# Kernel optimization log

Hardware: AMD Instinct MI355X
Metric: run time of the kernel (lower is better)

## Reference

```python
import jax, jax.numpy as jnp
import numpy as np

B, N, E, H, NE = 8, 512, 512, 8, 16384
DH = E // H
SCALE = DH ** -0.5
EPS = 1e-5


def _layernorm(x, g, b):
    mu = jnp.mean(x, axis=-1, keepdims=True)
    var = jnp.var(x, axis=-1, keepdims=True)
    return (x - mu) / jnp.sqrt(var + EPS) * g + b


def setup_inputs() -> dict:
    key = jax.random.key(0)
    ks = jax.random.split(key, 24)
    s = 0.02
    return {
        "x": jax.random.normal(ks[0], (B, N, E), jnp.float32),
        "edge_attr": jax.random.normal(ks[1], (NE, E), jnp.float32),
        "Wq": jax.random.normal(ks[2], (E, E), jnp.float32) * s,
        "bq": jnp.zeros((E,), jnp.float32),
        "Wk": jax.random.normal(ks[3], (E, E), jnp.float32) * s,
        "bk": jnp.zeros((E,), jnp.float32),
        "Wv": jax.random.normal(ks[4], (E, E), jnp.float32) * s,
        "bv": jnp.zeros((E,), jnp.float32),
        "Wo": jax.random.normal(ks[5], (E, E), jnp.float32) * s,
        "bo": jnp.zeros((E,), jnp.float32),
        "dist_table": jax.random.normal(ks[6], (100, H), jnp.float32),
        "We": jax.random.normal(ks[7], (H, E), jnp.float32) * s,
        "be": jnp.zeros((H,), jnp.float32),
        "W1": jax.random.normal(ks[8], (4 * E, E), jnp.float32) * s,
        "b1": jnp.zeros((4 * E,), jnp.float32),
        "W2": jax.random.normal(ks[9], (E, 4 * E), jnp.float32) * s,
        "b2": jnp.zeros((E,), jnp.float32),
        "g1": jnp.ones((E,), jnp.float32),
        "beta1": jnp.zeros((E,), jnp.float32),
        "g2": jnp.ones((E,), jnp.float32),
        "beta2": jnp.zeros((E,), jnp.float32),
        "edge_index": jax.random.randint(ks[10], (2, NE), 0, N, jnp.int64),
        "distance_matrix": jax.random.randint(ks[11], (B, N, N), 0, 100, jnp.int32),
    }


def reference(x, edge_attr, Wq, bq, Wk, bk, Wv, bv, Wo, bo, dist_table, We, be,
              W1, b1, W2, b2, g1, beta1, g2, beta2, edge_index, distance_matrix):
    residual = x
    h = _layernorm(x, g1, beta1)
    # projections -> [B, H, N, DH]
    def proj(W, b):
        return (h @ W.T + b).reshape(B, N, H, DH).transpose(0, 2, 1, 3)
    q, k, v = proj(Wq, bq), proj(Wk, bk), proj(Wv, bv)
    attn = jnp.einsum('bhnd,bhmd->bhnm', q, k) * SCALE
    # distance-encoding gather: [B,N,N] -> [B,N,N,H] -> [B,H,N,N]
    d_idx = jnp.clip(distance_matrix, 0, 99)
    attn = attn + dist_table[d_idx].transpose(0, 3, 1, 2)
    # per-edge scatter-add bias (duplicates accumulate, matching sequential loop)
    edge_enc = (edge_attr @ We.T + be).T  # [H, NE]
    src, tgt = edge_index[0], edge_index[1]
    edge_bias = jnp.zeros((H, N, N), attn.dtype).at[:, src, tgt].add(edge_enc)
    attn = attn + edge_bias[None]
    attn = jax.nn.softmax(attn, axis=-1)
    out = jnp.einsum('bhnm,bhmd->bhnd', attn, v)
    out = out.transpose(0, 2, 1, 3).reshape(B, N, E)
    out = out @ Wo.T + bo
    x1 = residual + out
    h2 = _layernorm(x1, g2, beta2)
    ffn = jax.nn.gelu(h2 @ W1.T + b1, approximate=False) @ W2.T + b2
    return x1 + ffn
```

## Files before the change

kernel.cpp:

```cpp
#include <hip/hip_runtime.h>
#include <cstdint>
#include <cstddef>

#define B_  8
#define N_  512
#define E_  512
#define H_  8
#define DH_ 64
#define NE_ 16384
#define QT  64

using u16   = unsigned short;
using bf16x8 = __attribute__((ext_vector_type(8))) __bf16;
using u16x8  = __attribute__((ext_vector_type(8))) unsigned short;
using f32x4  = __attribute__((ext_vector_type(4))) float;

__device__ __forceinline__ u16 f2b(float f) {
  unsigned u = __builtin_bit_cast(unsigned, f);
  u += 0x7fffu + ((u >> 16) & 1u);
  return (u16)(u >> 16);
}

__device__ __forceinline__ bf16x8 ld_frag(const u16* p) {
  return __builtin_bit_cast(bf16x8, *(const u16x8*)p);
}

__device__ __forceinline__ void gld_lds16(const u16* g, u16* l) {
  __builtin_amdgcn_global_load_lds(
      (const __attribute__((address_space(1))) unsigned*)(g),
      (__attribute__((address_space(3))) unsigned*)(l), 16, 0, 0);
}

__device__ __forceinline__ void gemm_core_128x128(
    const u16* __restrict__ At, int lda,
    const u16* __restrict__ Bt, int ldb, int K,
    u16* ldsA, u16* ldsB, f32x4 (&acc)[4][4]) {
  const int tid  = threadIdx.x;
  const int wid  = tid >> 6, lane = tid & 63;
  const int wr   = wid >> 1, wc = wid & 1;
  const int qd   = lane >> 4, r = lane & 15;
  const int mrow = tid >> 2, k0 = (tid & 3) * 8;
  const int wbase = wid << 9;
  for (int kt = 0; kt < K; kt += 32) {
    __syncthreads();
    gld_lds16(&At[(size_t)mrow*lda + kt + k0],        ldsA + wbase);
    gld_lds16(&At[(size_t)(mrow+64)*lda + kt + k0],   ldsA + 64*32 + wbase);
    gld_lds16(&Bt[(size_t)mrow*ldb + kt + k0],        ldsB + wbase);
    gld_lds16(&Bt[(size_t)(mrow+64)*ldb + kt + k0],   ldsB + 64*32 + wbase);
    __syncthreads();
    bf16x8 af[4], bfv[4];
#pragma unroll
    for (int i = 0; i < 4; ++i) af[i] = ld_frag(&ldsA[(wr*64 + i*16 + r)*32 + qd*8]);
#pragma unroll
    for (int j = 0; j < 4; ++j) bfv[j] = ld_frag(&ldsB[(wc*64 + j*16 + r)*32 + qd*8]);
#pragma unroll
    for (int i = 0; i < 4; ++i)
#pragma unroll
      for (int j = 0; j < 4; ++j)
        acc[i][j] = __builtin_amdgcn_mfma_f32_16x16x32_bf16(af[i], bfv[j], acc[i][j], 0, 0, 0);
  }
}

template <int EPI>
__global__ __launch_bounds__(256) void gemm_epi(
    const u16* __restrict__ A, const u16* __restrict__ W,
    const float* __restrict__ bias, const float* __restrict__ res,
    float* __restrict__ outf, u16* __restrict__ outb, int Kd, int Nd) {
  __shared__ u16 ldsA[128*32];
  __shared__ u16 ldsB[128*32];
  const int bx = blockIdx.x, by = blockIdx.y;
  f32x4 acc[4][4] = {};
  gemm_core_128x128(A + (size_t)bx*128*Kd, Kd, W + (size_t)by*128*Kd, Kd, Kd,
                    ldsA, ldsB, acc);
  const int tid = threadIdx.x, wid = tid>>6, lane = tid&63;
  const int wr = wid>>1, wc = wid&1, qd = lane>>4, r = lane&15;
#pragma unroll
  for (int i = 0; i < 4; ++i) {
#pragma unroll
    for (int j = 0; j < 4; ++j) {
      const int grow = bx*128 + wr*64 + i*16 + qd*4;
      const int gcol = by*128 + wc*64 + j*16 + r;
      const float bb = bias[gcol];
#pragma unroll
      for (int rg = 0; rg < 4; ++rg) {
        float v = acc[i][j][rg] + bb;
        const size_t idx = (size_t)(grow + rg)*Nd + gcol;
        if constexpr (EPI == 0) {
          outb[idx] = f2b(v);
        } else if constexpr (EPI == 1) {
          outf[idx] = v + res[idx];
        } else {
          v = 0.5f * v * (1.0f + erff(v * 0.70710678118f));
          outb[idx] = f2b(v);
        }
      }
    }
  }
}

__global__ __launch_bounds__(256) void gemm_splitk_k(
    const u16* __restrict__ A, const u16* __restrict__ W,
    float* __restrict__ part, int Kd, int Nd, int Ks) {
  __shared__ u16 ldsA[128*32];
  __shared__ u16 ldsB[128*32];
  const int bx = blockIdx.x, by = blockIdx.y, s = blockIdx.z;
  f32x4 acc[4][4] = {};
  gemm_core_128x128(A + (size_t)bx*128*Kd + (size_t)s*Ks, Kd,
                    W + (size_t)by*128*Kd + (size_t)s*Ks, Kd, Ks,
                    ldsA, ldsB, acc);
  const int tid = threadIdx.x, wid = tid>>6, lane = tid&63;
  const int wr = wid>>1, wc = wid&1, qd = lane>>4, r = lane&15;
  float* po = part + (size_t)s*(B_*N_)*Nd;
#pragma unroll
  for (int i = 0; i < 4; ++i) {
#pragma unroll
    for (int j = 0; j < 4; ++j) {
      const int grow = bx*128 + wr*64 + i*16 + qd*4;
      const int gcol = by*128 + wc*64 + j*16 + r;
#pragma unroll
      for (int rg = 0; rg < 4; ++rg)
        po[(size_t)(grow + rg)*Nd + gcol] = acc[i][j][rg];
    }
  }
}

template <int S>
__global__ __launch_bounds__(256) void splitk_reduce_k(
    const float* __restrict__ part, const float* __restrict__ bias,
    const float* __restrict__ res, float* __restrict__ out) {
  const size_t base = ((size_t)blockIdx.x*256 + threadIdx.x) * 4;
  float4 v = *(const float4*)&res[base];
  const int col = (int)(base & (E_-1));
  const float4 bb = *(const float4*)&bias[col];
  v.x += bb.x; v.y += bb.y; v.z += bb.z; v.w += bb.w;
#pragma unroll
  for (int s = 0; s < S; ++s) {
    const float4 p = *(const float4*)&part[(size_t)s*(B_*N_*E_) + base];
    v.x += p.x; v.y += p.y; v.z += p.z; v.w += p.w;
  }
  *(float4*)&out[base] = v;
}

__global__ __launch_bounds__(256) void qkv_gemm_k(
    const u16* __restrict__ A,
    const u16* __restrict__ Wqb, const u16* __restrict__ Wkb, const u16* __restrict__ Wvb,
    const float* __restrict__ bq, const float* __restrict__ bk, const float* __restrict__ bv,
    u16* __restrict__ qo, u16* __restrict__ ko, u16* __restrict__ vo) {
  __shared__ u16 ldsA[128*32];
  __shared__ u16 ldsB[128*32];
  const int bx = blockIdx.x, by = blockIdx.y, z = blockIdx.z;
  const u16*   W    = z == 0 ? Wqb : (z == 1 ? Wkb : Wvb);
  const float* bias = z == 0 ? bq  : (z == 1 ? bk  : bv);
  u16*         outb = z == 0 ? qo  : (z == 1 ? ko  : vo);
  f32x4 acc[4][4] = {};
  gemm_core_128x128(A + (size_t)bx*128*E_, E_, W + (size_t)by*128*E_, E_, E_,
                    ldsA, ldsB, acc);
  const int tid = threadIdx.x, wid = tid>>6, lane = tid&63;
  const int wr = wid>>1, wc = wid&1, qd = lane>>4, r = lane&15;
#pragma unroll
  for (int i = 0; i < 4; ++i) {
#pragma unroll
    for (int j = 0; j < 4; ++j) {
      const int grow = bx*128 + wr*64 + i*16 + qd*4;
      const int gcol = by*128 + wc*64 + j*16 + r;
      const float bb = bias[gcol];
#pragma unroll
      for (int rg = 0; rg < 4; ++rg)
        outb[(size_t)(grow + rg)*E_ + gcol] = f2b(acc[i][j][rg] + bb);
    }
  }
}

__global__ __launch_bounds__(256) void flash_attn_k(
    const u16* __restrict__ qm, const u16* __restrict__ km, const u16* __restrict__ vm,
    const float* __restrict__ dtab, const int* __restrict__ Dm,
    const float* __restrict__ ebias, u16* __restrict__ outb) {
  __shared__ u16 sQ[QT*72];
  __shared__ u16 sK[128*72];
  __shared__ u16 sP[QT*136];
  __shared__ u16 sVt[64*136];
  __shared__ float sDtab[100*H_];
  __shared__ float sMax[2][QT], sSum[2][QT], sM[QT], sL[QT], sAlpha[QT];

  const int bx = blockIdx.x;
  const int bz = blockIdx.y; const int b = bz>>3, h = bz&7;
  const int n0 = bx*QT;
  const int tid = threadIdx.x, wid = tid>>6, lane = tid&63;
  const int wr = wid>>1, wc = wid&1, qd = lane>>4, r = lane&15;

  {
    const u16* Qg = qm + ((size_t)(b*N_ + n0))*E_ + h*DH_;
#pragma unroll
    for (int it = 0; it < 2; ++it) {
      int idx = it*256 + tid;
      int row = idx>>3, d0 = (idx&7)*8;
      *(u16x8*)&sQ[row*72 + d0] = *(const u16x8*)&Qg[(size_t)row*E_ + d0];
    }
    for (int idx = tid; idx < 100*H_; idx += 256) sDtab[idx] = dtab[idx];
    if (tid < QT) { sM[tid] = -3.0e38f; sL[tid] = 0.f; }
  }

  f32x4 accO[2][2] = {};
  const int*   Db = Dm + (size_t)b*N_*N_;
  const float* Eb = ebias + (size_t)h*N_*N_;

  for (int mc = 0; mc < N_; mc += 128) {
    __syncthreads();
    {
      const u16* Kg = km + ((size_t)(b*N_ + mc))*E_ + h*DH_;
#pragma unroll
      for (int it = 0; it < 4; ++it) {
        int idx = it*256 + tid;
        int row = idx>>3, d0 = (idx&7)*8;
        *(u16x8*)&sK[row*72 + d0] = *(const u16x8*)&Kg[(size_t)row*E_ + d0];
      }
      const u16* Vg = vm + ((size_t)(b*N_ + mc))*E_ + h*DH_;
#pragma unroll
      for (int it = 0; it < 4; ++it) {
        int idx = it*256 + tid;
        int m = idx>>3, d0 = (idx&7)*8;
        u16x8 u = *(const u16x8*)&Vg[(size_t)m*E_ + d0];
#pragma unroll
        for (int e = 0; e < 8; ++e) sVt[(d0+e)*136 + m] = u[e];
      }
    }
    __syncthreads();
    f32x4 accS[2][4] = {};
#pragma unroll
    for (int ks = 0; ks < 2; ++ks) {
      bf16x8 af[2], bfv[4];
#pragma unroll
      for (int i = 0; i < 2; ++i) af[i] = ld_frag(&sQ[(wr*32 + i*16 + r)*72 + ks*32 + qd*8]);
#pragma unroll
      for (int j = 0; j < 4; ++j) bfv[j] = ld_frag(&sK[(wc*64 + j*16 + r)*72 + ks*32 + qd*8]);
#pragma unroll
      for (int i = 0; i < 2; ++i)
#pragma unroll
        for (int j = 0; j < 4; ++j)
          accS[i][j] = __builtin_amdgcn_mfma_f32_16x16x32_bf16(af[i], bfv[j], accS[i][j], 0, 0, 0);
    }
    float rmax[2][4];
#pragma unroll
    for (int i = 0; i < 2; ++i)
#pragma unroll
      for (int rg = 0; rg < 4; ++rg) rmax[i][rg] = -3.0e38f;
#pragma unroll
    for (int i = 0; i < 2; ++i) {
      const int n = n0 + wr*32 + i*16 + qd*4;
#pragma unroll
      for (int j = 0; j < 4; ++j) {
        const int m = mc + wc*64 + j*16 + r;
#pragma unroll
        for (int rg = 0; rg < 4; ++rg) {
          int di = Db[(size_t)(n+rg)*N_ + m];
          di = di < 0 ? 0 : (di > 99 ? 99 : di);
          float v = accS[i][j][rg]*0.125f + sDtab[di*H_ + h] + Eb[(size_t)(n+rg)*N_ + m];
          accS[i][j][rg] = v;
          rmax[i][rg] = fmaxf(rmax[i][rg], v);
        }
      }
    }
#pragma unroll
    for (int i = 0; i < 2; ++i)
#pragma unroll
      for (int rg = 0; rg < 4; ++rg) {
        float v = rmax[i][rg];
        v = fmaxf(v, __shfl_xor(v, 1)); v = fmaxf(v, __shfl_xor(v, 2));
        v = fmaxf(v, __shfl_xor(v, 4)); v = fmaxf(v, __shfl_xor(v, 8));
        if (r == 0) sMax[wc][wr*32 + i*16 + qd*4 + rg] = v;
      }
    __syncthreads();
    if (tid < QT) {
      float mcx  = fmaxf(sMax[0][tid], sMax[1][tid]);
      float mnew = fmaxf(sM[tid], mcx);
      sAlpha[tid] = __expf(sM[tid] - mnew);
      sM[tid] = mnew;
    }
    __syncthreads();
    float rsum[2][4];
#pragma unroll
    for (int i = 0; i < 2; ++i) {
      const int lr0 = wr*32 + i*16 + qd*4;
#pragma unroll
      for (int rg = 0; rg < 4; ++rg) {
        const float mrow = sM[lr0 + rg];
        float partial = 0.f;
#pragma unroll
        for (int j = 0; j < 4; ++j) {
          float p = __expf(accS[i][j][rg] - mrow);
          partial += p;
          sP[(lr0+rg)*136 + wc*64 + j*16 + r] = f2b(p);
        }
        rsum[i][rg] = partial;
        const float a = sAlpha[lr0 + rg];
#pragma unroll
        for (int jj = 0; jj < 2; ++jj) accO[i][jj][rg] *= a;
      }
    }
#pragma unroll
    for (int i = 0; i < 2; ++i)
#pragma unroll
      for (int rg = 0; rg < 4; ++rg) {
        float v = rsum[i][rg];
        v += __shfl_xor(v, 1); v += __shfl_xor(v, 2);
        v += __shfl_xor(v, 4); v += __shfl_xor(v, 8);
        if (r == 0) sSum[wc][wr*32 + i*16 + qd*4 + rg] = v;
      }
    __syncthreads();
    if (tid < QT) sL[tid] = sL[tid]*sAlpha[tid] + sSum[0][tid] + sSum[1][tid];
    __syncthreads();
#pragma unroll
    for (int ks = 0; ks < 4; ++ks) {
      bf16x8 af[2], bfv[2];
#pragma unroll
      for (int i = 0; i < 2; ++i) af[i] = ld_frag(&sP[(wr*32 + i*16 + r)*136 + ks*32 + qd*8]);
#pragma unroll
      for (int jj = 0; jj < 2; ++jj) bfv[jj] = ld_frag(&sVt[(wc*32 + jj*16 + r)*136 + ks*32 + qd*8]);
#pragma unroll
      for (int i = 0; i < 2; ++i)
#pragma unroll
        for (int jj = 0; jj < 2; ++jj)
          accO[i][jj] = __builtin_amdgcn_mfma_f32_16x16x32_bf16(af[i], bfv[jj], accO[i][jj], 0, 0, 0);
    }
  }
#pragma unroll
  for (int i = 0; i < 2; ++i) {
    const int lr0 = wr*32 + i*16 + qd*4;
#pragma unroll
    for (int jj = 0; jj < 2; ++jj) {
      const int d = wc*32 + jj*16 + r;
#pragma unroll
      for (int rg = 0; rg < 4; ++rg) {
        const float inv = 1.0f / sL[lr0 + rg];
        outb[((size_t)(b*N_ + n0 + lr0 + rg))*E_ + h*DH_ + d] = f2b(accO[i][jj][rg] * inv);
      }
    }
  }
}

__global__ __launch_bounds__(256) void layernorm_k(
    const float* __restrict__ x, const float* __restrict__ g,
    const float* __restrict__ be, u16* __restrict__ outb) {
  const int row = blockIdx.x, t = threadIdx.x;
  const float* xr = x + (size_t)row*E_;
  const float v0 = xr[t], v1 = xr[t+256];
  float s = v0 + v1, ss = v0*v0 + v1*v1;
  for (int o = 32; o; o >>= 1) { s += __shfl_down(s, o); ss += __shfl_down(ss, o); }
  __shared__ float rs[4], rss[4];
  const int wid = t>>6, lane = t&63;
  if (!lane) { rs[wid] = s; rss[wid] = ss; }
  __syncthreads();
  s  = rs[0]+rs[1]+rs[2]+rs[3];
  ss = rss[0]+rss[1]+rss[2]+rss[3];
  const float mu   = s * (1.0f/E_);
  const float var  = ss * (1.0f/E_) - mu*mu;
  const float rstd = rsqrtf(var + 1e-5f);
  outb[(size_t)row*E_ + t]       = f2b((v0-mu)*rstd*g[t] + be[t]);
  outb[(size_t)row*E_ + t + 256] = f2b((v1-mu)*rstd*g[t+256] + be[t+256]);
}

#define SEG0 32768
#define SEG1 65536
#define SEG2 98304
#define SEG3 131072
#define SEG4 262144
#define SEG5 393216
__global__ __launch_bounds__(256) void cvt_all_k(
    const float* __restrict__ Wq, const float* __restrict__ Wk,
    const float* __restrict__ Wv, const float* __restrict__ Wo,
    const float* __restrict__ W1, const float* __restrict__ W2,
    u16* __restrict__ wq_b, u16* __restrict__ wk_b, u16* __restrict__ wv_b,
    u16* __restrict__ wo_b, u16* __restrict__ w1_b, u16* __restrict__ w2_b) {
  const int i = blockIdx.x*256 + threadIdx.x;
  const float* src; u16* dst; int base;
  if      (i < SEG0) { src = Wq; dst = wq_b; base = 0; }
  else if (i < SEG1) { src = Wk; dst = wk_b; base = SEG0; }
  else if (i < SEG2) { src = Wv; dst = wv_b; base = SEG1; }
  else if (i < SEG3) { src = Wo; dst = wo_b; base = SEG2; }
  else if (i < SEG4) { src = W1; dst = w1_b; base = SEG3; }
  else               { src = W2; dst = w2_b; base = SEG4; }
  const int li = i - base;
  const float4 f0 = *(const float4*)&src[(size_t)li*8];
  const float4 f1 = *(const float4*)&src[(size_t)li*8 + 4];
  u16x8 u;
  u[0]=f2b(f0.x); u[1]=f2b(f0.y); u[2]=f2b(f0.z); u[3]=f2b(f0.w);
  u[4]=f2b(f1.x); u[5]=f2b(f1.y); u[6]=f2b(f1.z); u[7]=f2b(f1.w);
  *(u16x8*)&dst[(size_t)li*8] = u;
}

__global__ __launch_bounds__(256) void edge_enc_scatter_k(
    const float* __restrict__ ea, const float* __restrict__ We,
    const float* __restrict__ be, const int* __restrict__ ei,
    float* __restrict__ eb) {
  const int wglob = (blockIdx.x*256 + threadIdx.x) >> 6;
  const int lane  = threadIdx.x & 63;
  float w[8][8];
#pragma unroll
  for (int h = 0; h < 8; ++h) {
    const float4 f0 = *(const float4*)&We[h*E_ + lane*8];
    const float4 f1 = *(const float4*)&We[h*E_ + lane*8 + 4];
    w[h][0]=f0.x; w[h][1]=f0.y; w[h][2]=f0.z; w[h][3]=f0.w;
    w[h][4]=f1.x; w[h][5]=f1.y; w[h][6]=f1.z; w[h][7]=f1.w;
  }
  const float beh = (lane < 8) ? be[lane] : 0.f;
#pragma unroll 1
  for (int t = 0; t < NE_/2048; ++t) {
    const int e = wglob*(NE_/2048) + t;
    const float* ar = ea + (size_t)e*E_;
    const float4 a0 = *(const float4*)&ar[lane*8];
    const float4 a1 = *(const float4*)&ar[lane*8 + 4];
    const float a[8] = {a0.x,a0.y,a0.z,a0.w,a1.x,a1.y,a1.z,a1.w};
    float acc[8];
#pragma unroll
    for (int h = 0; h < 8; ++h) {
      float s = 0.f;
#pragma unroll
      for (int j = 0; j < 8; ++j) s += a[j]*w[h][j];
      acc[h] = s;
    }
#pragma unroll
    for (int h = 0; h < 8; ++h) {
      float v = acc[h];
      v += __shfl_xor(v, 1);  v += __shfl_xor(v, 2);  v += __shfl_xor(v, 4);
      v += __shfl_xor(v, 8);  v += __shfl_xor(v, 16); v += __shfl_xor(v, 32);
      acc[h] = v;
    }
    float myv = acc[0];
#pragma unroll
    for (int h = 1; h < 8; ++h) myv = (lane == h) ? acc[h] : myv;
    if (lane < 8) {
      const int s2 = ei[e], t2 = ei[NE_ + e];
      atomicAdd(&eb[((size_t)lane*N_ + s2)*N_ + t2], myv + beh);
    }
  }
}

extern "C" void kernel_launch(void* const* d_in, const int* in_sizes, int n_in,
                              void* d_out, int out_size, void* d_ws, size_t ws_size,
                              hipStream_t stream) {
  const float* x     = (const float*)d_in[0];
  const float* ea    = (const float*)d_in[1];
  const float* Wq    = (const float*)d_in[2];
  const float* bq    = (const float*)d_in[3];
  const float* Wk    = (const float*)d_in[4];
  const float* bk    = (const float*)d_in[5];
  const float* Wv    = (const float*)d_in[6];
  const float* bv    = (const float*)d_in[7];
  const float* Wo    = (const float*)d_in[8];
  const float* bo    = (const float*)d_in[9];
  const float* dtab  = (const float*)d_in[10];
  const float* We    = (const float*)d_in[11];
  const float* be    = (const float*)d_in[12];
  const float* W1    = (const float*)d_in[13];
  const float* b1    = (const float*)d_in[14];
  const float* W2    = (const float*)d_in[15];
  const float* b2    = (const float*)d_in[16];
  const float* g1    = (const float*)d_in[17];
  const float* bet1  = (const float*)d_in[18];
  const float* g2    = (const float*)d_in[19];
  const float* bet2  = (const float*)d_in[20];
  const int*   eidx  = (const int*)d_in[21];
  const int*   Dmat  = (const int*)d_in[22];
  float* out = (float*)d_out;

  char* ws = (char*)d_ws;
  size_t off = 0;
  auto alloc = [&](size_t bytes) -> void* {
    void* p = ws + off;
    off += (bytes + 255) & ~(size_t)255;
    return p;
  };
  u16* wq_b = (u16*)alloc((size_t)E_*E_*2);
  u16* wk_b = (u16*)alloc((size_t)E_*E_*2);
  u16* wv_b = (u16*)alloc((size_t)E_*E_*2);
  u16* wo_b = (u16*)alloc((size_t)E_*E_*2);
  u16* w1_b = (u16*)alloc((size_t)4*E_*E_*2);
  u16* w2_b = (u16*)alloc((size_t)4*E_*E_*2);
  u16* h_b  = (u16*)alloc((size_t)B_*N_*E_*2);
  u16* q_b  = (u16*)alloc((size_t)B_*N_*E_*2);
  u16* k_b  = (u16*)alloc((size_t)B_*N_*E_*2);
  u16* v_b  = (u16*)alloc((size_t)B_*N_*E_*2);
  float* ebias = (float*)alloc((size_t)H_*N_*N_*4);
  float* x1    = (float*)alloc((size_t)B_*N_*E_*4);
  u16*   h2_b  = (u16*)alloc((size_t)B_*N_*E_*2);
  u16*   mid_b = (u16*)alloc((size_t)B_*N_*4*E_*2);
  float* part  = (float*)alloc((size_t)4*B_*N_*E_*4);
  u16*   ao_b  = h_b;

  const int M = B_*N_;

  cvt_all_k<<<dim3(SEG5/256), 256, 0, stream>>>(
      Wq, Wk, Wv, Wo, W1, W2, wq_b, wk_b, wv_b, wo_b, w1_b, w2_b);

  layernorm_k<<<dim3(M), 256, 0, stream>>>(x, g1, bet1, h_b);

  qkv_gemm_k<<<dim3(M/128, E_/128, 3), 256, 0, stream>>>(
      h_b, wq_b, wk_b, wv_b, bq, bk, bv, q_b, k_b, v_b);

  hipMemsetAsync(ebias, 0, (size_t)H_*N_*N_*4, stream);
  edge_enc_scatter_k<<<dim3(512), 256, 0, stream>>>(ea, We, be, eidx, ebias);

  flash_attn_k<<<dim3(N_/QT, B_*H_), 256, 0, stream>>>(
      q_b, k_b, v_b, dtab, Dmat, ebias, ao_b);

  gemm_splitk_k<<<dim3(M/128, E_/128, 2), 256, 0, stream>>>(
      ao_b, wo_b, part, E_, E_, E_/2);
  splitk_reduce_k<2><<<dim3(M*E_/1024), 256, 0, stream>>>(part, bo, x, x1);

  layernorm_k<<<dim3(M), 256, 0, stream>>>(x1, g2, bet2, h2_b);

  gemm_epi<2><<<dim3(M/128, 4*E_/128), 256, 0, stream>>>(h2_b, w1_b, b1, nullptr, nullptr, mid_b, E_, 4*E_);

  gemm_splitk_k<<<dim3(M/128, E_/128, 4), 256, 0, stream>>>(
      mid_b, w2_b, part, 4*E_, E_, E_);
  splitk_reduce_k<4><<<dim3(M*E_/1024), 256, 0, stream>>>(part, b2, x1, out);
}
```

Measured before the change: 280.1 us.

## Fuse layernorms into neighbours and restructure flash attention loads and softmax state

Merges the weight conversion and first layernorm into one launch, and fuses the Wo split-K reduction with the second layernorm. Flash attention now loads Q/K through direct global-to-LDS copies in a k-split layout and prefetches distance and edge-bias values into registers before the barrier. It keeps the running max and sum per thread in registers, removing two block barriers per tile, and staggers the V-transpose and P stores to reduce LDS bank conflicts. This adds register pressure (32 prefetched values per thread), which may lower occupancy.

```diff
diff --git a/kernel.cpp b/kernel.cpp
--- a/kernel.cpp
+++ b/kernel.cpp
@@ -141,6 +141,42 @@
   *(float4*)&out[base] = v;
 }
 
+__device__ __forceinline__ void ln_store(
+    float v0, float v1, const float* __restrict__ g,
+    const float* __restrict__ be, u16* __restrict__ outb, int row, int t) {
+  float s = v0 + v1, ss = v0*v0 + v1*v1;
+  for (int o = 32; o; o >>= 1) { s += __shfl_down(s, o); ss += __shfl_down(ss, o); }
+  __shared__ float rs[4], rss[4];
+  const int wid = t>>6, lane = t&63;
+  if (!lane) { rs[wid] = s; rss[wid] = ss; }
+  __syncthreads();
+  s  = rs[0]+rs[1]+rs[2]+rs[3];
+  ss = rss[0]+rss[1]+rss[2]+rss[3];
+  const float mu   = s * (1.0f/E_);
+  const float var  = ss * (1.0f/E_) - mu*mu;
+  const float rstd = rsqrtf(var + 1e-5f);
+  outb[(size_t)row*E_ + t]       = f2b((v0-mu)*rstd*g[t] + be[t]);
+  outb[(size_t)row*E_ + t + 256] = f2b((v1-mu)*rstd*g[t+256] + be[t+256]);
+}
+
+__global__ __launch_bounds__(256) void splitk_reduce_ln_k(
+    const float* __restrict__ part, const float* __restrict__ bias,
+    const float* __restrict__ res, float* __restrict__ x1,
+    const float* __restrict__ g, const float* __restrict__ be,
+    u16* __restrict__ h2b) {
+  const int row = blockIdx.x, t = threadIdx.x;
+  const size_t base = (size_t)row*E_;
+  float v0 = res[base + t]       + bias[t];
+  float v1 = res[base + t + 256] + bias[t + 256];
+#pragma unroll
+  for (int s = 0; s < 2; ++s) {
+    v0 += part[(size_t)s*(B_*N_*E_) + base + t];
+    v1 += part[(size_t)s*(B_*N_*E_) + base + t + 256];
+  }
+  x1[base + t] = v0; x1[base + t + 256] = v1;
+  ln_store(v0, v1, g, be, h2b, row, t);
+}
+
 __global__ __launch_bounds__(256) void qkv_gemm_k(
     const u16* __restrict__ A,
     const u16* __restrict__ Wqb, const u16* __restrict__ Wkb, const u16* __restrict__ Wvb,
@@ -175,53 +211,75 @@
     const u16* __restrict__ qm, const u16* __restrict__ km, const u16* __restrict__ vm,
     const float* __restrict__ dtab, const int* __restrict__ Dm,
     const float* __restrict__ ebias, u16* __restrict__ outb) {
-  __shared__ u16 sQ[QT*72];
-  __shared__ u16 sK[128*72];
-  __shared__ u16 sP[QT*136];
+  __shared__ u16 sQ[2*64*32];
+  __shared__ u16 sK[2*128*32];
+  __shared__ u16 sP[64*136];
   __shared__ u16 sVt[64*136];
-  __shared__ float sDtab[100*H_];
-  __shared__ float sMax[2][QT], sSum[2][QT], sM[QT], sL[QT], sAlpha[QT];
+  __shared__ float sDt[104];
+  __shared__ float sMax[2][64], sSum[2][64];
 
   const int bx = blockIdx.x;
   const int bz = blockIdx.y; const int b = bz>>3, h = bz&7;
   const int n0 = bx*QT;
   const int tid = threadIdx.x, wid = tid>>6, lane = tid&63;
   const int wr = wid>>1, wc = wid&1, qd = lane>>4, r = lane&15;
-
-  {
-    const u16* Qg = qm + ((size_t)(b*N_ + n0))*E_ + h*DH_;
-#pragma unroll
-    for (int it = 0; it < 2; ++it) {
-      int idx = it*256 + tid;
-      int row = idx>>3, d0 = (idx&7)*8;
-      *(u16x8*)&sQ[row*72 + d0] = *(const u16x8*)&Qg[(size_t)row*E_ + d0];
-    }
-    for (int idx = tid; idx < 100*H_; idx += 256) sDtab[idx] = dtab[idx];
-    if (tid < QT) { sM[tid] = -3.0e38f; sL[tid] = 0.f; }
-  }
-
-  f32x4 accO[2][2] = {};
+  const int lrow = lane>>2, lk = (lane&3)*8;
+
+  const u16* Qg = qm + ((size_t)(b*N_ + n0))*E_ + h*DH_;
+  const u16* Kg = km + (size_t)b*N_*E_ + h*DH_;
+  const u16* Vg = vm + (size_t)b*N_*E_ + h*DH_;
   const int*   Db = Dm + (size_t)b*N_*N_;
   const float* Eb = ebias + (size_t)h*N_*N_;
 
+  {
+#pragma unroll
+    for (int ks = 0; ks < 2; ++ks)
+      gld_lds16(&Qg[(size_t)(wid*16 + lrow)*E_ + ks*32 + lk],
+                sQ + ks*2048 + wid*16*32);
+    for (int idx = tid; idx < 100; idx += 256) sDt[idx] = dtab[idx*H_ + h];
+  }
+
+  float mI[2][4], lI[2][4], alph[2][4];
+#pragma unroll
+  for (int i = 0; i < 2; ++i)
+#pragma unroll
+    for (int rg = 0; rg < 4; ++rg) { mI[i][rg] = -3.0e38f; lI[i][rg] = 0.f; }
+  f32x4 accO[2][2] = {};
+
   for (int mc = 0; mc < N_; mc += 128) {
+    int   dpre[2][4][4];
+    float epre[2][4][4];
+#pragma unroll
+    for (int i = 0; i < 2; ++i) {
+      const int nb = n0 + wr*32 + i*16 + qd*4;
+#pragma unroll
+      for (int j = 0; j < 4; ++j) {
+        const int m = mc + wc*64 + j*16 + r;
+#pragma unroll
+        for (int rg = 0; rg < 4; ++rg) {
+          dpre[i][j][rg] = Db[(size_t)(nb+rg)*N_ + m];
+          epre[i][j][rg] = Eb[(size_t)(nb+rg)*N_ + m];
+        }
+      }
+    }
     __syncthreads();
-    {
-      const u16* Kg = km + ((size_t)(b*N_ + mc))*E_ + h*DH_;
-#pragma unroll
-      for (int it = 0; it < 4; ++it) {
-        int idx = it*256 + tid;
-        int row = idx>>3, d0 = (idx&7)*8;
-        *(u16x8*)&sK[row*72 + d0] = *(const u16x8*)&Kg[(size_t)row*E_ + d0];
-      }
-      const u16* Vg = vm + ((size_t)(b*N_ + mc))*E_ + h*DH_;
-#pragma unroll
-      for (int it = 0; it < 4; ++it) {
-        int idx = it*256 + tid;
-        int m = idx>>3, d0 = (idx&7)*8;
-        u16x8 u = *(const u16x8*)&Vg[(size_t)m*E_ + d0];
-#pragma unroll
-        for (int e = 0; e < 8; ++e) sVt[(d0+e)*136 + m] = u[e];
+#pragma unroll
+    for (int t = 0; t < 2; ++t) {
+      const int row0 = wid*32 + t*16;
+#pragma unroll
+      for (int ks = 0; ks < 2; ++ks)
+        gld_lds16(&Kg[(size_t)(mc + row0 + lrow)*E_ + ks*32 + lk],
+                  sK + ks*4096 + row0*32);
+    }
+#pragma unroll
+    for (int it = 0; it < 4; ++it) {
+      const int idx = it*256 + tid;
+      const int m = idx>>3, d0 = (idx&7)*8;
+      const u16x8 u = *(const u16x8*)&Vg[(size_t)(mc+m)*E_ + d0];
+#pragma unroll
+      for (int e = 0; e < 8; ++e) {
+        const int pe = (e + (d0>>3)) & 7;
+        sVt[(d0+pe)*136 + m] = u[pe];
       }
     }
     __syncthreads();
@@ -230,9 +288,11 @@
     for (int ks = 0; ks < 2; ++ks) {
       bf16x8 af[2], bfv[4];
 #pragma unroll
-      for (int i = 0; i < 2; ++i) af[i] = ld_frag(&sQ[(wr*32 + i*16 + r)*72 + ks*32 + qd*8]);
-#pragma unroll
-      for (int j = 0; j < 4; ++j) bfv[j] = ld_frag(&sK[(wc*64 + j*16 + r)*72 + ks*32 + qd*8]);
+      for (int i = 0; i < 2; ++i)
+        af[i] = ld_frag(&sQ[ks*2048 + (wr*32 + i*16 + r)*32 + qd*8]);
+#pragma unroll
+      for (int j = 0; j < 4; ++j)
+        bfv[j] = ld_frag(&sK[ks*4096 + (wc*64 + j*16 + r)*32 + qd*8]);
 #pragma unroll
       for (int i = 0; i < 2; ++i)
 #pragma unroll
@@ -245,21 +305,17 @@
 #pragma unroll
       for (int rg = 0; rg < 4; ++rg) rmax[i][rg] = -3.0e38f;
 #pragma unroll
-    for (int i = 0; i < 2; ++i) {
-      const int n = n0 + wr*32 + i*16 + qd*4;
-#pragma unroll
-      for (int j = 0; j < 4; ++j) {
-        const int m = mc + wc*64 + j*16 + r;
+    for (int i = 0; i < 2; ++i)
+#pragma unroll
+      for (int j = 0; j < 4; ++j)
 #pragma unroll
         for (int rg = 0; rg < 4; ++rg) {
-          int di = Db[(size_t)(n+rg)*N_ + m];
+          int di = dpre[i][j][rg];
           di = di < 0 ? 0 : (di > 99 ? 99 : di);
-          float v = accS[i][j][rg]*0.125f + sDtab[di*H_ + h] + Eb[(size_t)(n+rg)*N_ + m];
+          const float v = accS[i][j][rg]*0.125f + sDt[di] + epre[i][j][rg];
           accS[i][j][rg] = v;
           rmax[i][rg] = fmaxf(rmax[i][rg], v);
         }
-      }
-    }
 #pragma unroll
     for (int i = 0; i < 2; ++i)
 #pragma unroll
@@ -270,31 +326,32 @@
         if (r == 0) sMax[wc][wr*32 + i*16 + qd*4 + rg] = v;
       }
     __syncthreads();
-    if (tid < QT) {
-      float mcx  = fmaxf(sMax[0][tid], sMax[1][tid]);
-      float mnew = fmaxf(sM[tid], mcx);
-      sAlpha[tid] = __expf(sM[tid] - mnew);
-      sM[tid] = mnew;
-    }
-    __syncthreads();
+#pragma unroll
+    for (int i = 0; i < 2; ++i)
+#pragma unroll
+      for (int rg = 0; rg < 4; ++rg) {
+        const int row = wr*32 + i*16 + qd*4 + rg;
+        const float mx   = fmaxf(sMax[0][row], sMax[1][row]);
+        const float mnew = fmaxf(mI[i][rg], mx);
+        alph[i][rg] = __expf(mI[i][rg] - mnew);
+        mI[i][rg]   = mnew;
+      }
     float rsum[2][4];
 #pragma unroll
     for (int i = 0; i < 2; ++i) {
       const int lr0 = wr*32 + i*16 + qd*4;
 #pragma unroll
       for (int rg = 0; rg < 4; ++rg) {
-        const float mrow = sM[lr0 + rg];
+        const float mrow = mI[i][rg];
         float partial = 0.f;
 #pragma unroll
-        for (int j = 0; j < 4; ++j) {
-          float p = __expf(accS[i][j][rg] - mrow);
+        for (int jj0 = 0; jj0 < 4; ++jj0) {
+          const int j = (jj0 + qd) & 3;
+          const float p = __expf(accS[i][j][rg] - mrow);
           partial += p;
           sP[(lr0+rg)*136 + wc*64 + j*16 + r] = f2b(p);
         }
         rsum[i][rg] = partial;
-        const float a = sAlpha[lr0 + rg];
-#pragma unroll
-        for (int jj = 0; jj < 2; ++jj) accO[i][jj][rg] *= a;
       }
     }
 #pragma unroll
@@ -305,17 +362,26 @@
         v += __shfl_xor(v, 1); v += __shfl_xor(v, 2);
         v += __shfl_xor(v, 4); v += __shfl_xor(v, 8);
         if (r == 0) sSum[wc][wr*32 + i*16 + qd*4 + rg] = v;
+#pragma unroll
+        for (int jj = 0; jj < 2; ++jj) accO[i][jj][rg] *= alph[i][rg];
       }
     __syncthreads();
-    if (tid < QT) sL[tid] = sL[tid]*sAlpha[tid] + sSum[0][tid] + sSum[1][tid];
-    __syncthreads();
+#pragma unroll
+    for (int i = 0; i < 2; ++i)
+#pragma unroll
+      for (int rg = 0; rg < 4; ++rg) {
+        const int row = wr*32 + i*16 + qd*4 + rg;
+        lI[i][rg] = lI[i][rg]*alph[i][rg] + sSum[0][row] + sSum[1][row];
+      }
 #pragma unroll
     for (int ks = 0; ks < 4; ++ks) {
       bf16x8 af[2], bfv[2];
 #pragma unroll
-      for (int i = 0; i < 2; ++i) af[i] = ld_frag(&sP[(wr*32 + i*16 + r)*136 + ks*32 + qd*8]);
-#pragma unroll
-      for (int jj = 0; jj < 2; ++jj) bfv[jj] = ld_frag(&sVt[(wc*32 + jj*16 + r)*136 + ks*32 + qd*8]);
+      for (int i = 0; i < 2; ++i)
+        af[i] = ld_frag(&sP[(wr*32 + i*16 + r)*136 + ks*32 + qd*8]);
+#pragma unroll
+      for (int jj = 0; jj < 2; ++jj)
+        bfv[jj] = ld_frag(&sVt[(wc*32 + jj*16 + r)*136 + ks*32 + qd*8]);
 #pragma unroll
       for (int i = 0; i < 2; ++i)
 #pragma unroll
@@ -331,32 +397,11 @@
       const int d = wc*32 + jj*16 + r;
 #pragma unroll
       for (int rg = 0; rg < 4; ++rg) {
-        const float inv = 1.0f / sL[lr0 + rg];
+        const float inv = 1.0f / lI[i][rg];
         outb[((size_t)(b*N_ + n0 + lr0 + rg))*E_ + h*DH_ + d] = f2b(accO[i][jj][rg] * inv);
       }
     }
   }
-}
-
-__global__ __launch_bounds__(256) void layernorm_k(
-    const float* __restrict__ x, const float* __restrict__ g,
-    const float* __restrict__ be, u16* __restrict__ outb) {
-  const int row = blockIdx.x, t = threadIdx.x;
-  const float* xr = x + (size_t)row*E_;
-  const float v0 = xr[t], v1 = xr[t+256];
-  float s = v0 + v1, ss = v0*v0 + v1*v1;
-  for (int o = 32; o; o >>= 1) { s += __shfl_down(s, o); ss += __shfl_down(ss, o); }
-  __shared__ float rs[4], rss[4];
-  const int wid = t>>6, lane = t&63;
-  if (!lane) { rs[wid] = s; rss[wid] = ss; }
-  __syncthreads();
-  s  = rs[0]+rs[1]+rs[2]+rs[3];
-  ss = rss[0]+rss[1]+rss[2]+rss[3];
-  const float mu   = s * (1.0f/E_);
-  const float var  = ss * (1.0f/E_) - mu*mu;
-  const float rstd = rsqrtf(var + 1e-5f);
-  outb[(size_t)row*E_ + t]       = f2b((v0-mu)*rstd*g[t] + be[t]);
-  outb[(size_t)row*E_ + t + 256] = f2b((v1-mu)*rstd*g[t+256] + be[t+256]);
 }
 
 #define SEG0 32768
@@ -365,27 +410,35 @@
 #define SEG3 131072
 #define SEG4 262144
 #define SEG5 393216
-__global__ __launch_bounds__(256) void cvt_all_k(
+__global__ __launch_bounds__(256) void prep_k(
     const float* __restrict__ Wq, const float* __restrict__ Wk,
     const float* __restrict__ Wv, const float* __restrict__ Wo,
     const float* __restrict__ W1, const float* __restrict__ W2,
     u16* __restrict__ wq_b, u16* __restrict__ wk_b, u16* __restrict__ wv_b,
-    u16* __restrict__ wo_b, u16* __restrict__ w1_b, u16* __restrict__ w2_b) {
-  const int i = blockIdx.x*256 + threadIdx.x;
-  const float* src; u16* dst; int base;
-  if      (i < SEG0) { src = Wq; dst = wq_b; base = 0; }
-  else if (i < SEG1) { src = Wk; dst = wk_b; base = SEG0; }
-  else if (i < SEG2) { src = Wv; dst = wv_b; base = SEG1; }
-  else if (i < SEG3) { src = Wo; dst = wo_b; base = SEG2; }
-  else if (i < SEG4) { src = W1; dst = w1_b; base = SEG3; }
-  else               { src = W2; dst = w2_b; base = SEG4; }
-  const int li = i - base;
-  const float4 f0 = *(const float4*)&src[(size_t)li*8];
-  const float4 f1 = *(const float4*)&src[(size_t)li*8 + 4];
-  u16x8 u;
-  u[0]=f2b(f0.x); u[1]=f2b(f0.y); u[2]=f2b(f0.z); u[3]=f2b(f0.w);
-  u[4]=f2b(f1.x); u[5]=f2b(f1.y); u[6]=f2b(f1.z); u[7]=f2b(f1.w);
-  *(u16x8*)&dst[(size_t)li*8] = u;
+    u16* __restrict__ wo_b, u16* __restrict__ w1_b, u16* __restrict__ w2_b,
+    const float* __restrict__ x, const float* __restrict__ g1,
+    const float* __restrict__ bet1, u16* __restrict__ h_b) {
+  if (blockIdx.x < 1536) {
+    const int i = blockIdx.x*256 + threadIdx.x;
+    const float* src; u16* dst; int base;
+    if      (i < SEG0) { src = Wq; dst = wq_b; base = 0; }
+    else if (i < SEG1) { src = Wk; dst = wk_b; base = SEG0; }
+    else if (i < SEG2) { src = Wv; dst = wv_b; base = SEG1; }
+    else if (i < SEG3) { src = Wo; dst = wo_b; base = SEG2; }
+    else if (i < SEG4) { src = W1; dst = w1_b; base = SEG3; }
+    else               { src = W2; dst = w2_b; base = SEG4; }
+    const int li = i - base;
+    const float4 f0 = *(const float4*)&src[(size_t)li*8];
+    const float4 f1 = *(const float4*)&src[(size_t)li*8 + 4];
+    u16x8 u;
+    u[0]=f2b(f0.x); u[1]=f2b(f0.y); u[2]=f2b(f0.z); u[3]=f2b(f0.w);
+    u[4]=f2b(f1.x); u[5]=f2b(f1.y); u[6]=f2b(f1.z); u[7]=f2b(f1.w);
+    *(u16x8*)&dst[(size_t)li*8] = u;
+  } else {
+    const int row = blockIdx.x - 1536, t = threadIdx.x;
+    const float v0 = x[(size_t)row*E_ + t], v1 = x[(size_t)row*E_ + t + 256];
+    ln_store(v0, v1, g1, bet1, h_b, row, t);
+  }
 }
 
 __global__ __launch_bounds__(256) void edge_enc_scatter_k(
@@ -489,10 +542,9 @@
 
   const int M = B_*N_;
 
-  cvt_all_k<<<dim3(SEG5/256), 256, 0, stream>>>(
-      Wq, Wk, Wv, Wo, W1, W2, wq_b, wk_b, wv_b, wo_b, w1_b, w2_b);
-
-  layernorm_k<<<dim3(M), 256, 0, stream>>>(x, g1, bet1, h_b);
+  prep_k<<<dim3(1536 + M), 256, 0, stream>>>(
+      Wq, Wk, Wv, Wo, W1, W2, wq_b, wk_b, wv_b, wo_b, w1_b, w2_b,
+      x, g1, bet1, h_b);
 
   qkv_gemm_k<<<dim3(M/128, E_/128, 3), 256, 0, stream>>>(
       h_b, wq_b, wk_b, wv_b, bq, bk, bv, q_b, k_b, v_b);
@@ -505,9 +557,8 @@
 
   gemm_splitk_k<<<dim3(M/128, E_/128, 2), 256, 0, stream>>>(
       ao_b, wo_b, part, E_, E_, E_/2);
-  splitk_reduce_k<2><<<dim3(M*E_/1024), 256, 0, stream>>>(part, bo, x, x1);
-
-  layernorm_k<<<dim3(M), 256, 0, stream>>>(x1, g2, bet2, h2_b);
+  splitk_reduce_ln_k<<<dim3(M), 256, 0, stream>>>(
+      part, bo, x, x1, g2, bet2, h2_b);
 
   gemm_epi<2><<<dim3(M/128, 4*E_/128), 256, 0, stream>>>(h2_b, w1_b, b1, nullptr, nullptr, mid_b, E_, 4*E_);
 
```

Measured after the change: 329.1 us. +17.5%, slower.
